# Kernel tuning notes

Hardware: AMD Instinct MI355X
Metric: run time of the kernel (lower is better)

The kernel has to match this reference:

```python
import jax, jax.numpy as jnp
import numpy as np

D_MODEL = 768
N_HEAD = 12
D_FF = 3072
EPS = 1e-5


def _layer_norm(x, w, b):
    mu = jnp.mean(x, axis=-1, keepdims=True)
    var = jnp.mean(jnp.square(x - mu), axis=-1, keepdims=True)
    return (x - mu) * jax.lax.rsqrt(var + EPS) * w + b


def setup_inputs() -> dict:
    key = jax.random.key(0)
    ks = jax.random.split(key, 8)
    B, S, D = 2, 4096, D_MODEL
    s_in = 1.0 / np.sqrt(D)
    s_ff = 1.0 / np.sqrt(D_FF)
    return {
        "src": jax.random.normal(ks[0], (B, S, D), jnp.float32),
        "w_qkv": jax.random.uniform(ks[1], (3 * D, D), jnp.float32, -s_in, s_in),
        "b_qkv": jnp.zeros((3 * D,), jnp.float32),
        "w_out": jax.random.uniform(ks[2], (D, D), jnp.float32, -s_in, s_in),
        "b_out": jnp.zeros((D,), jnp.float32),
        "w1": jax.random.uniform(ks[3], (D_FF, D), jnp.float32, -s_in, s_in),
        "b1": jnp.zeros((D_FF,), jnp.float32),
        "w2": jax.random.uniform(ks[4], (D, D_FF), jnp.float32, -s_ff, s_ff),
        "b2": jnp.zeros((D,), jnp.float32),
        "ln1_w": jnp.ones((D,), jnp.float32),
        "ln1_b": jnp.zeros((D,), jnp.float32),
        "ln2_w": jnp.ones((D,), jnp.float32),
        "ln2_b": jnp.zeros((D,), jnp.float32),
    }


def reference(src, w_qkv, b_qkv, w_out, b_out, w1, b1, w2, b2,
              ln1_w, ln1_b, ln2_w, ln2_b):
    B, S, D = src.shape
    H, dh = N_HEAD, D // N_HEAD
    # fused QKV projection: [B,S,3D]
    qkv = jnp.einsum('bsd,ed->bse', src, w_qkv) + b_qkv
    q, k, v = jnp.split(qkv, 3, axis=-1)
    q = q.reshape(B, S, H, dh)
    k = k.reshape(B, S, H, dh)
    v = v.reshape(B, S, H, dh)
    scale = 1.0 / np.sqrt(dh)
    scores = jnp.einsum('bqhd,bkhd->bhqk', q, k) * scale  # [B,H,S,S]
    attn = jax.nn.softmax(scores, axis=-1)
    ctx = jnp.einsum('bhqk,bkhd->bqhd', attn, v).reshape(B, S, D)
    attn_out = jnp.einsum('bsd,ed->bse', ctx, w_out) + b_out
    # post-norm residual (norm_first=False), dropout inactive in eval
    x = _layer_norm(src + attn_out, ln1_w, ln1_b)
    h = jax.nn.relu(jnp.einsum('bsd,fd->bsf', x, w1) + b1)
    ffn = jnp.einsum('bsf,df->bsd', h, w2) + b2
    return _layer_norm(x + ffn, ln2_w, ln2_b)
```

## Files before the change

kernel.cpp:

```cpp
#include <hip/hip_runtime.h>
#include <hip/hip_bf16.h>

typedef __hip_bfloat16 bf16;
typedef __attribute__((ext_vector_type(8))) short s16x8;
typedef __attribute__((ext_vector_type(4))) float f32x4;

#define MFMA16x16x32(A, B, C) __builtin_amdgcn_mfma_f32_16x16x32_bf16((A), (B), (C), 0, 0, 0)

__device__ __forceinline__ void async_copy16(const bf16* g, bf16* l) {
  __builtin_amdgcn_global_load_lds(
      (const __attribute__((address_space(1))) void*)g,
      (__attribute__((address_space(3))) void*)l, 16, 0, 0);
}

__device__ __forceinline__ int SW(int row, int chunk) {
  return row * 64 + (((chunk) ^ (row & 7)) << 3);
}

__global__ __launch_bounds__(256)
void cast_f2b_kernel(const float* __restrict__ in, bf16* __restrict__ out, int n) {
  const int i = (blockIdx.x * 256 + threadIdx.x) * 4;
  if (i < n) {
    const float4 f = *(const float4*)(in + i);
    out[i + 0] = (bf16)f.x; out[i + 1] = (bf16)f.y;
    out[i + 2] = (bf16)f.z; out[i + 3] = (bf16)f.w;
  }
}

template <int RELU, int VT, int ACCUM, typename OutT>
__global__ __launch_bounds__(256)
void gemm_bt_kernel(const bf16* __restrict__ A, const bf16* __restrict__ B,
                    const float* __restrict__ bias, OutT* __restrict__ C,
                    int N, int K, int ldb, bf16* __restrict__ C2) {
  __shared__ __align__(16) bf16 As[2][128 * 32];
  __shared__ __align__(16) bf16 Bs[2][128 * 32];

  const int t = threadIdx.x;
  const int lane = t & 63;
  const int wave = t >> 6;
  const int wm = (wave >> 1) << 6;
  const int wn = (wave & 1) << 6;
  const int col16 = lane & 15;
  const int quad = lane >> 4;
  const int bm = blockIdx.x;
  const int bn = blockIdx.y;

  const bf16* Ag = A + (size_t)(bm * 128 + (t >> 2)) * K + (t & 3) * 8;
  const bf16* Bg = B + (size_t)(bn * 128 + (t >> 2)) * ldb + (t & 3) * 8;

  f32x4 acc[4][4] = {};

  async_copy16(Ag, &As[0][0] + t * 8);
  async_copy16(Ag + (size_t)64 * K, &As[0][0] + 2048 + t * 8);
  async_copy16(Bg, &Bs[0][0] + t * 8);
  async_copy16(Bg + (size_t)64 * ldb, &Bs[0][0] + 2048 + t * 8);

  int n = 0;
  for (int k0 = 0; k0 < K; k0 += 32, n ^= 1) {
    __syncthreads();
    if (k0 + 32 < K) {
      const int k1 = k0 + 32;
      async_copy16(Ag + k1, &As[n ^ 1][0] + t * 8);
      async_copy16(Ag + (size_t)64 * K + k1, &As[n ^ 1][0] + 2048 + t * 8);
      async_copy16(Bg + k1, &Bs[n ^ 1][0] + t * 8);
      async_copy16(Bg + (size_t)64 * ldb + k1, &Bs[n ^ 1][0] + 2048 + t * 8);
    }
    const bf16* asn = &As[n][0];
    const bf16* bsn = &Bs[n][0];

    s16x8 af[4], bfr[4];
#pragma unroll
    for (int i = 0; i < 4; i++)
      af[i] = *(const s16x8*)(asn + (wm + i * 16 + col16) * 32 + quad * 8);
#pragma unroll
    for (int j = 0; j < 4; j++)
      bfr[j] = *(const s16x8*)(bsn + (wn + j * 16 + col16) * 32 + quad * 8);
#pragma unroll
    for (int i = 0; i < 4; i++)
#pragma unroll
      for (int j = 0; j < 4; j++)
        acc[i][j] = MFMA16x16x32(af[i], bfr[j], acc[i][j]);
  }

  const int row0 = bm * 128 + wm + quad * 4;
  const int col0 = bn * 128 + wn + col16;
#pragma unroll
  for (int j = 0; j < 4; j++) {
    const int col = col0 + j * 16;
    const float bv = ACCUM ? 0.0f : bias[col];
#pragma unroll
    for (int i = 0; i < 4; i++) {
#pragma unroll
      for (int r = 0; r < 4; r++) {
        float v = acc[i][j][r] + bv;
        if (RELU) v = fmaxf(v, 0.0f);
        const int row = row0 + i * 16 + r;
        if (VT == 1) {
          ((bf16*)C)[(size_t)((row >> 12) * 12 + (col >> 6)) * 262144 +
                     (col & 63) * 4096 + (row & 4095)] = (bf16)v;
        } else if (VT == 2) {
          if (col < 1536) {
            C[(size_t)row * N + col] = (OutT)v;
          } else {
            const int cc = col - 1536;
            C2[(size_t)((row >> 12) * 12 + (cc >> 6)) * 262144 +
               (cc & 63) * 4096 + (row & 4095)] = (bf16)v;
          }
        } else {
          const size_t idx = (size_t)row * N + col;
          if (ACCUM) v += ((const float*)C)[idx];
          C[idx] = (OutT)v;
        }
      }
    }
  }
}

__global__ __launch_bounds__(256)
void attn_kernel(const bf16* __restrict__ QK, const bf16* __restrict__ Vt,
                 bf16* __restrict__ Opart, float* __restrict__ lbuf) {
  __shared__ __align__(16) bf16 Ks[2][64 * 64];
  __shared__ __align__(16) bf16 Vs[2][64 * 64];
  __shared__ __align__(16) bf16 Ps[4][32 * 64];

  const int t = threadIdx.x, lane = t & 63, wave = t >> 6;
  const int col16 = lane & 15, quad = lane >> 4;
  const int b = blockIdx.z, h = blockIdx.y;
  const int ks = blockIdx.x >> 5;
  const int qblk = blockIdx.x & 31;
  const int qw0 = qblk * 128 + wave * 32;

  s16x8 bq[2][2];
#pragma unroll
  for (int qt = 0; qt < 2; qt++)
#pragma unroll
    for (int s = 0; s < 2; s++) {
      union { s16x8 v; bf16 hh[8]; } u;
      u.v = *(const s16x8*)(QK + (size_t)(b * 4096 + qw0 + qt * 16 + col16) * 1536 +
                            h * 64 + s * 32 + quad * 8);
#pragma unroll
      for (int e = 0; e < 8; e++) u.hh[e] = (bf16)((float)u.hh[e] * 0.18033688f);
      bq[qt][s] = u.v;
    }

  union { s16x8 v; short s_[8]; } uo1;
#pragma unroll
  for (int e = 0; e < 8; e++) uo1.s_[e] = (short)0x3F80;
  const s16x8 aones = uo1.v;

  const int srow = t >> 3;
  const int schx = (t & 7) ^ (srow & 7);
  const bf16* kgb = QK + (size_t)(b * 4096) * 1536 + 768 + h * 64;
  const bf16* vgb = Vt + (size_t)(b * 12 + h) * 262144;
  const bf16* ksrc0 = kgb + (size_t)srow * 1536 + schx * 8;
  const bf16* ksrc1 = kgb + (size_t)(32 + srow) * 1536 + schx * 8;
  const bf16* vsrc0 = vgb + (size_t)srow * 4096 + schx * 8;
  const bf16* vsrc1 = vgb + (size_t)(32 + srow) * 4096 + schx * 8;

  f32x4 o[4][2] = {};
  f32x4 lacc[2] = {};
  bf16* pw = &Ps[wave][0];

  const int kbeg = ks * 2048, kend = kbeg + 2048;

  async_copy16(ksrc0 + (size_t)kbeg * 1536, &Ks[0][0] + t * 8);
  async_copy16(ksrc1 + (size_t)kbeg * 1536, &Ks[0][0] + 2048 + t * 8);
  async_copy16(vsrc0 + kbeg, &Vs[0][0] + t * 8);
  async_copy16(vsrc1 + kbeg, &Vs[0][0] + 2048 + t * 8);

  int n = 0;
  for (int k0 = kbeg; k0 < kend; k0 += 64, n ^= 1) {
    __syncthreads();
    if (k0 + 64 < kend) {
      const int k1 = k0 + 64;
      async_copy16(ksrc0 + (size_t)k1 * 1536, &Ks[n ^ 1][0] + t * 8);
      async_copy16(ksrc1 + (size_t)k1 * 1536, &Ks[n ^ 1][0] + 2048 + t * 8);
      async_copy16(vsrc0 + k1, &Vs[n ^ 1][0] + t * 8);
      async_copy16(vsrc1 + k1, &Vs[n ^ 1][0] + 2048 + t * 8);
    }
    const bf16* ksn = &Ks[n][0];
    const bf16* vsn = &Vs[n][0];

    f32x4 st[4][2] = {};
#pragma unroll
    for (int s = 0; s < 2; s++) {
      s16x8 ak[4];
#pragma unroll
      for (int kt = 0; kt < 4; kt++)
        ak[kt] = *(const s16x8*)(ksn + SW(kt * 16 + col16, s * 4 + quad));
#pragma unroll
      for (int kt = 0; kt < 4; kt++)
#pragma unroll
        for (int qt = 0; qt < 2; qt++)
          st[kt][qt] = MFMA16x16x32(ak[kt], bq[qt][s], st[kt][qt]);
    }

#pragma unroll
    for (int qt = 0; qt < 2; qt++) {
#pragma unroll
      for (int kt = 0; kt < 4; kt++) {
        union { unsigned long long u; bf16 hh[4]; } pk;
#pragma unroll
        for (int r = 0; r < 4; r++)
          pk.hh[r] = (bf16)__builtin_amdgcn_exp2f(st[kt][qt][r]);
        *(unsigned long long*)(pw + (qt * 16 + col16) * 64 +
                               (((kt * 2 + (quad >> 1)) ^ (col16 & 7)) << 3) +
                               (quad & 1) * 4) = pk.u;
      }
    }
    asm volatile("s_waitcnt lgkmcnt(0)" ::: "memory");

#pragma unroll
    for (int s = 0; s < 2; s++) {
      s16x8 bp[2];
#pragma unroll
      for (int qt = 0; qt < 2; qt++)
        bp[qt] = *(const s16x8*)(pw + SW(qt * 16 + col16, s * 4 + quad));
#pragma unroll
      for (int qt = 0; qt < 2; qt++)
        lacc[qt] = MFMA16x16x32(aones, bp[qt], lacc[qt]);
#pragma unroll
      for (int dt = 0; dt < 4; dt++) {
        const s16x8 av = *(const s16x8*)(vsn + SW(dt * 16 + col16, s * 4 + quad));
#pragma unroll
        for (int qt = 0; qt < 2; qt++)
          o[dt][qt] = MFMA16x16x32(av, bp[qt], o[dt][qt]);
      }
    }
  }

  if (lane < 16) {
#pragma unroll
    for (int qt = 0; qt < 2; qt++)
      lbuf[(size_t)ks * 98304 + (size_t)(b * 4096 + qw0 + qt * 16 + lane) * 12 + h] =
          lacc[qt][0];
  }

#pragma unroll
  for (int qt = 0; qt < 2; qt++)
#pragma unroll
    for (int dt = 0; dt < 4; dt++)
#pragma unroll
      for (int r = 0; r < 4; r++)
        pw[(qt * 16 + col16) * 64 + (((dt * 2 + (quad >> 1)) ^ (col16 & 7)) << 3) +
           (quad & 1) * 4 + r] = (bf16)(o[dt][qt][r]);
  asm volatile("s_waitcnt lgkmcnt(0)" ::: "memory");
  const int qrow = lane >> 1, chalf = (lane & 1) * 4;
  bf16* dst = Opart + (size_t)ks * 6291456 +
              (size_t)(b * 4096 + qw0 + qrow) * 768 + h * 64 + chalf * 8;
#pragma unroll
  for (int i = 0; i < 4; i++)
    *(s16x8*)(dst + i * 8) = *(const s16x8*)(pw + SW(qrow, chalf + i));
}

__global__ __launch_bounds__(256)
void attn_combine_kernel(const bf16* __restrict__ Opart,
                         const float* __restrict__ lbuf,
                         bf16* __restrict__ ctx) {
  const int i = blockIdx.x * 256 + threadIdx.x;
  const int row = i / 96, c8 = i % 96;
  const int h = c8 >> 3;
  const float inv = 1.0f / (lbuf[(size_t)row * 12 + h] +
                            lbuf[98304 + (size_t)row * 12 + h]);
  union { s16x8 v; bf16 hh[8]; } ua, ub, uo;
  ua.v = *(const s16x8*)(Opart + (size_t)row * 768 + c8 * 8);
  ub.v = *(const s16x8*)(Opart + 6291456 + (size_t)row * 768 + c8 * 8);
#pragma unroll
  for (int j = 0; j < 8; j++)
    uo.hh[j] = (bf16)(((float)ua.hh[j] + (float)ub.hh[j]) * inv);
  *(s16x8*)(ctx + (size_t)row * 768 + c8 * 8) = uo.v;
}

__global__ __launch_bounds__(256)
void add_ln_b_kernel(const float* __restrict__ X, const float* __restrict__ Y,
                     const float* __restrict__ w, const float* __restrict__ b,
                     bf16* __restrict__ out) {
  const int row = blockIdx.x * 4 + (threadIdx.x >> 6);
  const int lane = threadIdx.x & 63;
  const float* x = X + (size_t)row * 768;
  const float* y = Y + (size_t)row * 768;
  float v[12];
  float s = 0.0f;
#pragma unroll
  for (int i = 0; i < 3; i++) {
    const int c = lane * 4 + i * 256;
    const float4 xf = *(const float4*)(x + c);
    const float4 yf = *(const float4*)(y + c);
    v[i * 4 + 0] = xf.x + yf.x; v[i * 4 + 1] = xf.y + yf.y;
    v[i * 4 + 2] = xf.z + yf.z; v[i * 4 + 3] = xf.w + yf.w;
    s += v[i * 4] + v[i * 4 + 1] + v[i * 4 + 2] + v[i * 4 + 3];
  }
#pragma unroll
  for (int off = 32; off > 0; off >>= 1) s += __shfl_xor(s, off, 64);
  const float mu = s * (1.0f / 768.0f);
  float var = 0.0f;
#pragma unroll
  for (int i = 0; i < 12; i++) { const float d = v[i] - mu; var += d * d; }
#pragma unroll
  for (int off = 32; off > 0; off >>= 1) var += __shfl_xor(var, off, 64);
  const float rs = rsqrtf(var * (1.0f / 768.0f) + 1e-5f);
#pragma unroll
  for (int i = 0; i < 12; i++) {
    const int c = lane * 4 + (i >> 2) * 256 + (i & 3);
    out[(size_t)row * 768 + c] = (bf16)((v[i] - mu) * rs * w[c] + b[c]);
  }
}

__global__ __launch_bounds__(256)
void add_ln_f_kernel(const bf16* __restrict__ X, const float* __restrict__ Y,
                     const float* __restrict__ w, const float* __restrict__ b,
                     float* __restrict__ out) {
  const int row = blockIdx.x * 4 + (threadIdx.x >> 6);
  const int lane = threadIdx.x & 63;
  const bf16* x = X + (size_t)row * 768;
  const float* y = Y + (size_t)row * 768;
  float v[12];
  float s = 0.0f;
#pragma unroll
  for (int i = 0; i < 3; i++) {
    const int c = lane * 4 + i * 256;
    const float4 yf = *(const float4*)(y + c);
    v[i * 4 + 0] = (float)x[c + 0] + yf.x; v[i * 4 + 1] = (float)x[c + 1] + yf.y;
    v[i * 4 + 2] = (float)x[c + 2] + yf.z; v[i * 4 + 3] = (float)x[c + 3] + yf.w;
    s += v[i * 4] + v[i * 4 + 1] + v[i * 4 + 2] + v[i * 4 + 3];
  }
#pragma unroll
  for (int off = 32; off > 0; off >>= 1) s += __shfl_xor(s, off, 64);
  const float mu = s * (1.0f / 768.0f);
  float var = 0.0f;
#pragma unroll
  for (int i = 0; i < 12; i++) { const float d = v[i] - mu; var += d * d; }
#pragma unroll
  for (int off = 32; off > 0; off >>= 1) var += __shfl_xor(var, off, 64);
  const float rs = rsqrtf(var * (1.0f / 768.0f) + 1e-5f);
#pragma unroll
  for (int i = 0; i < 12; i++) {
    const int c = lane * 4 + (i >> 2) * 256 + (i & 3);
    out[(size_t)row * 768 + c] = (v[i] - mu) * rs * w[c] + b[c];
  }
}

extern "C" void kernel_launch(void* const* d_in, const int* in_sizes, int n_in,
                              void* d_out, int out_size, void* d_ws, size_t ws_size,
                              hipStream_t stream) {
  (void)in_sizes; (void)n_in; (void)out_size; (void)ws_size;
  const float* src   = (const float*)d_in[0];
  const float* w_qkv = (const float*)d_in[1];
  const float* b_qkv = (const float*)d_in[2];
  const float* w_out = (const float*)d_in[3];
  const float* b_out = (const float*)d_in[4];
  const float* w1    = (const float*)d_in[5];
  const float* b1    = (const float*)d_in[6];
  const float* w2    = (const float*)d_in[7];
  const float* b2    = (const float*)d_in[8];
  const float* ln1w  = (const float*)d_in[9];
  const float* ln1b  = (const float*)d_in[10];
  const float* ln2w  = (const float*)d_in[11];
  const float* ln2b  = (const float*)d_in[12];
  float* out = (float*)d_out;

  char* ws = (char*)d_ws;
  bf16* wqkvb = (bf16*)ws;
  bf16* woutb = (bf16*)(ws + 3538944);
  bf16* w1b   = (bf16*)(ws + 4718592);
  bf16* w2b   = (bf16*)(ws + 9437184);
  bf16* srcb  = (bf16*)(ws + 14155776);
  bf16* QK    = (bf16*)(ws + 26738688);
  bf16* Vt    = (bf16*)(ws + 51904512);
  bf16* Opart = (bf16*)d_out;
  float* lbuf = (float*)ws;
  bf16* ctx   = (bf16*)(ws + 14155776);
  float* attn_out = (float*)(ws + 26738688);
  bf16* x1b   = (bf16*)(ws + 51904512);
  bf16* hbuf  = (bf16*)(ws + 14155776);
  float* ffn  = out;

  cast_f2b_kernel<<<1728, 256, 0, stream>>>(w_qkv, wqkvb, 2304 * 768);
  cast_f2b_kernel<<<576,  256, 0, stream>>>(w_out, woutb, 768 * 768);
  cast_f2b_kernel<<<2304, 256, 0, stream>>>(w1, w1b, 3072 * 768);
  cast_f2b_kernel<<<2304, 256, 0, stream>>>(w2, w2b, 768 * 3072);
  cast_f2b_kernel<<<6144, 256, 0, stream>>>(src, srcb, 8192 * 768);

  gemm_bt_kernel<0, 2, 0, bf16><<<dim3(64, 18), 256, 0, stream>>>(
      srcb, wqkvb, b_qkv, QK, 1536, 768, 768, Vt);
  attn_kernel<<<dim3(64, 12, 2), 256, 0, stream>>>(QK, Vt, Opart, lbuf);
  attn_combine_kernel<<<3072, 256, 0, stream>>>(Opart, lbuf, ctx);
  gemm_bt_kernel<0, 0, 0, float><<<dim3(64, 6), 256, 0, stream>>>(
      ctx, woutb, b_out, attn_out, 768, 768, 768, nullptr);
  add_ln_b_kernel<<<2048, 256, 0, stream>>>(src, attn_out, ln1w, ln1b, x1b);
  for (int c = 0; c < 2; c++) {
    gemm_bt_kernel<1, 0, 0, bf16><<<dim3(64, 12), 256, 0, stream>>>(
        x1b, w1b + (size_t)c * 1536 * 768, b1 + c * 1536, hbuf, 1536, 768, 768,
        nullptr);
    if (c == 0)
      gemm_bt_kernel<0, 0, 0, float><<<dim3(64, 6), 256, 0, stream>>>(
          hbuf, w2b + c * 1536, b2, ffn, 768, 1536, 3072, nullptr);
    else
      gemm_bt_kernel<0, 0, 1, float><<<dim3(64, 6), 256, 0, stream>>>(
          hbuf, w2b + c * 1536, b2, ffn, 768, 1536, 3072, nullptr);
  }
  add_ln_f_kernel<<<2048, 256, 0, stream>>>(x1b, ffn, ln2w, ln2b, out);
}
```

Before: 498.1 us.

## Enlarge attention query tile, split-K the out-projection, and merge cast launches

The attention kernel now gives each wave 64 query rows instead of 32, doubling the block's query tile to 256. Each loaded K/V tile is reused across more queries, at the cost of more registers, a larger P buffer in shared memory, and half as many blocks. The output projection is split along K into two halves written to separate buffers, which doubles its grid, and the layer-norm kernel sums both partials. The five cast kernels are fused into one launch to cut launch overhead.

```diff
diff --git a/kernel.cpp b/kernel.cpp
--- a/kernel.cpp
+++ b/kernel.cpp
@@ -18,20 +18,29 @@
 }
 
 __global__ __launch_bounds__(256)
-void cast_f2b_kernel(const float* __restrict__ in, bf16* __restrict__ out, int n) {
-  const int i = (blockIdx.x * 256 + threadIdx.x) * 4;
-  if (i < n) {
-    const float4 f = *(const float4*)(in + i);
-    out[i + 0] = (bf16)f.x; out[i + 1] = (bf16)f.y;
-    out[i + 2] = (bf16)f.z; out[i + 3] = (bf16)f.w;
-  }
+void cast_all_kernel(const float* __restrict__ s0, bf16* __restrict__ d0,
+                     const float* __restrict__ s1, bf16* __restrict__ d1,
+                     const float* __restrict__ s2, bf16* __restrict__ d2,
+                     const float* __restrict__ s3, bf16* __restrict__ d3,
+                     const float* __restrict__ s4, bf16* __restrict__ d4) {
+  int blk = blockIdx.x;
+  const float* in; bf16* out;
+  if (blk < 1728)      { in = s0; out = d0; }
+  else if (blk < 2304) { in = s1; out = d1; blk -= 1728; }
+  else if (blk < 4608) { in = s2; out = d2; blk -= 2304; }
+  else if (blk < 6912) { in = s3; out = d3; blk -= 4608; }
+  else                 { in = s4; out = d4; blk -= 6912; }
+  const int i = (blk * 256 + threadIdx.x) * 4;
+  const float4 f = *(const float4*)(in + i);
+  out[i + 0] = (bf16)f.x; out[i + 1] = (bf16)f.y;
+  out[i + 2] = (bf16)f.z; out[i + 3] = (bf16)f.w;
 }
 
 template <int RELU, int VT, int ACCUM, typename OutT>
 __global__ __launch_bounds__(256)
 void gemm_bt_kernel(const bf16* __restrict__ A, const bf16* __restrict__ B,
                     const float* __restrict__ bias, OutT* __restrict__ C,
-                    int N, int K, int ldb, bf16* __restrict__ C2) {
+                    int N, int K, int lda, int ldb, bf16* __restrict__ C2) {
   __shared__ __align__(16) bf16 As[2][128 * 32];
   __shared__ __align__(16) bf16 Bs[2][128 * 32];
 
@@ -44,14 +53,15 @@
   const int quad = lane >> 4;
   const int bm = blockIdx.x;
   const int bn = blockIdx.y;
-
-  const bf16* Ag = A + (size_t)(bm * 128 + (t >> 2)) * K + (t & 3) * 8;
-  const bf16* Bg = B + (size_t)(bn * 128 + (t >> 2)) * ldb + (t & 3) * 8;
+  const int kz = (VT == 3) ? blockIdx.z * K : 0;
+
+  const bf16* Ag = A + (size_t)(bm * 128 + (t >> 2)) * lda + (t & 3) * 8 + kz;
+  const bf16* Bg = B + (size_t)(bn * 128 + (t >> 2)) * ldb + (t & 3) * 8 + kz;
 
   f32x4 acc[4][4] = {};
 
   async_copy16(Ag, &As[0][0] + t * 8);
-  async_copy16(Ag + (size_t)64 * K, &As[0][0] + 2048 + t * 8);
+  async_copy16(Ag + (size_t)64 * lda, &As[0][0] + 2048 + t * 8);
   async_copy16(Bg, &Bs[0][0] + t * 8);
   async_copy16(Bg + (size_t)64 * ldb, &Bs[0][0] + 2048 + t * 8);
 
@@ -61,7 +71,7 @@
     if (k0 + 32 < K) {
       const int k1 = k0 + 32;
       async_copy16(Ag + k1, &As[n ^ 1][0] + t * 8);
-      async_copy16(Ag + (size_t)64 * K + k1, &As[n ^ 1][0] + 2048 + t * 8);
+      async_copy16(Ag + (size_t)64 * lda + k1, &As[n ^ 1][0] + 2048 + t * 8);
       async_copy16(Bg + k1, &Bs[n ^ 1][0] + t * 8);
       async_copy16(Bg + (size_t)64 * ldb + k1, &Bs[n ^ 1][0] + 2048 + t * 8);
     }
@@ -87,7 +97,7 @@
 #pragma unroll
   for (int j = 0; j < 4; j++) {
     const int col = col0 + j * 16;
-    const float bv = ACCUM ? 0.0f : bias[col];
+    const float bv = (ACCUM || (VT == 3 && blockIdx.z)) ? 0.0f : bias[col];
 #pragma unroll
     for (int i = 0; i < 4; i++) {
 #pragma unroll
@@ -95,10 +105,7 @@
         float v = acc[i][j][r] + bv;
         if (RELU) v = fmaxf(v, 0.0f);
         const int row = row0 + i * 16 + r;
-        if (VT == 1) {
-          ((bf16*)C)[(size_t)((row >> 12) * 12 + (col >> 6)) * 262144 +
-                     (col & 63) * 4096 + (row & 4095)] = (bf16)v;
-        } else if (VT == 2) {
+        if (VT == 2) {
           if (col < 1536) {
             C[(size_t)row * N + col] = (OutT)v;
           } else {
@@ -106,6 +113,8 @@
             C2[(size_t)((row >> 12) * 12 + (cc >> 6)) * 262144 +
                (cc & 63) * 4096 + (row & 4095)] = (bf16)v;
           }
+        } else if (VT == 3) {
+          ((float*)(blockIdx.z ? (void*)C2 : (void*)C))[(size_t)row * N + col] = v;
         } else {
           const size_t idx = (size_t)row * N + col;
           if (ACCUM) v += ((const float*)C)[idx];
@@ -116,23 +125,23 @@
   }
 }
 
-__global__ __launch_bounds__(256)
+__global__ __launch_bounds__(256, 2)
 void attn_kernel(const bf16* __restrict__ QK, const bf16* __restrict__ Vt,
                  bf16* __restrict__ Opart, float* __restrict__ lbuf) {
   __shared__ __align__(16) bf16 Ks[2][64 * 64];
   __shared__ __align__(16) bf16 Vs[2][64 * 64];
-  __shared__ __align__(16) bf16 Ps[4][32 * 64];
+  __shared__ __align__(16) bf16 Ps[4][64 * 64];
 
   const int t = threadIdx.x, lane = t & 63, wave = t >> 6;
   const int col16 = lane & 15, quad = lane >> 4;
   const int b = blockIdx.z, h = blockIdx.y;
-  const int ks = blockIdx.x >> 5;
-  const int qblk = blockIdx.x & 31;
-  const int qw0 = qblk * 128 + wave * 32;
-
-  s16x8 bq[2][2];
-#pragma unroll
-  for (int qt = 0; qt < 2; qt++)
+  const int ks = blockIdx.x >> 4;
+  const int qblk = blockIdx.x & 15;
+  const int qw0 = qblk * 256 + wave * 64;
+
+  s16x8 bq[4][2];
+#pragma unroll
+  for (int qt = 0; qt < 4; qt++)
 #pragma unroll
     for (int s = 0; s < 2; s++) {
       union { s16x8 v; bf16 hh[8]; } u;
@@ -157,8 +166,8 @@
   const bf16* vsrc0 = vgb + (size_t)srow * 4096 + schx * 8;
   const bf16* vsrc1 = vgb + (size_t)(32 + srow) * 4096 + schx * 8;
 
-  f32x4 o[4][2] = {};
-  f32x4 lacc[2] = {};
+  f32x4 o[4][4] = {};
+  f32x4 lacc[4] = {};
   bf16* pw = &Ps[wave][0];
 
   const int kbeg = ks * 2048, kend = kbeg + 2048;
@@ -181,28 +190,27 @@
     const bf16* ksn = &Ks[n][0];
     const bf16* vsn = &Vs[n][0];
 
-    f32x4 st[4][2] = {};
-#pragma unroll
-    for (int s = 0; s < 2; s++) {
-      s16x8 ak[4];
+    s16x8 ak[2][4];
+#pragma unroll
+    for (int s = 0; s < 2; s++)
 #pragma unroll
       for (int kt = 0; kt < 4; kt++)
-        ak[kt] = *(const s16x8*)(ksn + SW(kt * 16 + col16, s * 4 + quad));
-#pragma unroll
-      for (int kt = 0; kt < 4; kt++)
-#pragma unroll
-        for (int qt = 0; qt < 2; qt++)
-          st[kt][qt] = MFMA16x16x32(ak[kt], bq[qt][s], st[kt][qt]);
-    }
-
-#pragma unroll
-    for (int qt = 0; qt < 2; qt++) {
-#pragma unroll
-      for (int kt = 0; kt < 4; kt++) {
+        ak[s][kt] = *(const s16x8*)(ksn + SW(kt * 16 + col16, s * 4 + quad));
+
+#pragma unroll
+    for (int kt = 0; kt < 4; kt++) {
+      f32x4 st[4] = {};
+#pragma unroll
+      for (int s = 0; s < 2; s++)
+#pragma unroll
+        for (int qt = 0; qt < 4; qt++)
+          st[qt] = MFMA16x16x32(ak[s][kt], bq[qt][s], st[qt]);
+#pragma unroll
+      for (int qt = 0; qt < 4; qt++) {
         union { unsigned long long u; bf16 hh[4]; } pk;
 #pragma unroll
         for (int r = 0; r < 4; r++)
-          pk.hh[r] = (bf16)__builtin_amdgcn_exp2f(st[kt][qt][r]);
+          pk.hh[r] = (bf16)__builtin_amdgcn_exp2f(st[qt][r]);
         *(unsigned long long*)(pw + (qt * 16 + col16) * 64 +
                                (((kt * 2 + (quad >> 1)) ^ (col16 & 7)) << 3) +
                                (quad & 1) * 4) = pk.u;
@@ -212,18 +220,18 @@
 
 #pragma unroll
     for (int s = 0; s < 2; s++) {
-      s16x8 bp[2];
-#pragma unroll
-      for (int qt = 0; qt < 2; qt++)
+      s16x8 bp[4];
+#pragma unroll
+      for (int qt = 0; qt < 4; qt++)
         bp[qt] = *(const s16x8*)(pw + SW(qt * 16 + col16, s * 4 + quad));
 #pragma unroll
-      for (int qt = 0; qt < 2; qt++)
+      for (int qt = 0; qt < 4; qt++)
         lacc[qt] = MFMA16x16x32(aones, bp[qt], lacc[qt]);
 #pragma unroll
       for (int dt = 0; dt < 4; dt++) {
         const s16x8 av = *(const s16x8*)(vsn + SW(dt * 16 + col16, s * 4 + quad));
 #pragma unroll
-        for (int qt = 0; qt < 2; qt++)
+        for (int qt = 0; qt < 4; qt++)
           o[dt][qt] = MFMA16x16x32(av, bp[qt], o[dt][qt]);
       }
     }
@@ -231,13 +239,13 @@
 
   if (lane < 16) {
 #pragma unroll
-    for (int qt = 0; qt < 2; qt++)
+    for (int qt = 0; qt < 4; qt++)
       lbuf[(size_t)ks * 98304 + (size_t)(b * 4096 + qw0 + qt * 16 + lane) * 12 + h] =
           lacc[qt][0];
   }
 
 #pragma unroll
-  for (int qt = 0; qt < 2; qt++)
+  for (int qt = 0; qt < 4; qt++)
 #pragma unroll
     for (int dt = 0; dt < 4; dt++)
 #pragma unroll
@@ -246,11 +254,15 @@
            (quad & 1) * 4 + r] = (bf16)(o[dt][qt][r]);
   asm volatile("s_waitcnt lgkmcnt(0)" ::: "memory");
   const int qrow = lane >> 1, chalf = (lane & 1) * 4;
-  bf16* dst = Opart + (size_t)ks * 6291456 +
-              (size_t)(b * 4096 + qw0 + qrow) * 768 + h * 64 + chalf * 8;
-#pragma unroll
-  for (int i = 0; i < 4; i++)
-    *(s16x8*)(dst + i * 8) = *(const s16x8*)(pw + SW(qrow, chalf + i));
+#pragma unroll
+  for (int h2 = 0; h2 < 2; h2++) {
+    const int rl = h2 * 32 + qrow;
+    bf16* dst = Opart + (size_t)ks * 6291456 +
+                (size_t)(b * 4096 + qw0 + rl) * 768 + h * 64 + chalf * 8;
+#pragma unroll
+    for (int i = 0; i < 4; i++)
+      *(s16x8*)(dst + i * 8) = *(const s16x8*)(pw + SW(rl, chalf + i));
+  }
 }
 
 __global__ __launch_bounds__(256)
@@ -273,12 +285,14 @@
 
 __global__ __launch_bounds__(256)
 void add_ln_b_kernel(const float* __restrict__ X, const float* __restrict__ Y,
+                     const float* __restrict__ Y2,
                      const float* __restrict__ w, const float* __restrict__ b,
                      bf16* __restrict__ out) {
   const int row = blockIdx.x * 4 + (threadIdx.x >> 6);
   const int lane = threadIdx.x & 63;
   const float* x = X + (size_t)row * 768;
   const float* y = Y + (size_t)row * 768;
+  const float* y2 = Y2 + (size_t)row * 768;
   float v[12];
   float s = 0.0f;
 #pragma unroll
@@ -286,8 +300,9 @@
     const int c = lane * 4 + i * 256;
     const float4 xf = *(const float4*)(x + c);
     const float4 yf = *(const float4*)(y + c);
-    v[i * 4 + 0] = xf.x + yf.x; v[i * 4 + 1] = xf.y + yf.y;
-    v[i * 4 + 2] = xf.z + yf.z; v[i * 4 + 3] = xf.w + yf.w;
+    const float4 zf = *(const float4*)(y2 + c);
+    v[i * 4 + 0] = xf.x + yf.x + zf.x; v[i * 4 + 1] = xf.y + yf.y + zf.y;
+    v[i * 4 + 2] = xf.z + yf.z + zf.z; v[i * 4 + 3] = xf.w + yf.w + zf.w;
     s += v[i * 4] + v[i * 4 + 1] + v[i * 4 + 2] + v[i * 4 + 3];
   }
 #pragma unroll
@@ -370,34 +385,32 @@
   bf16* Opart = (bf16*)d_out;
   float* lbuf = (float*)ws;
   bf16* ctx   = (bf16*)(ws + 14155776);
-  float* attn_out = (float*)(ws + 26738688);
+  float* woP0 = (float*)(ws + 26738688);
+  float* woP1 = (float*)d_out;
   bf16* x1b   = (bf16*)(ws + 51904512);
   bf16* hbuf  = (bf16*)(ws + 14155776);
   float* ffn  = out;
 
-  cast_f2b_kernel<<<1728, 256, 0, stream>>>(w_qkv, wqkvb, 2304 * 768);
-  cast_f2b_kernel<<<576,  256, 0, stream>>>(w_out, woutb, 768 * 768);
-  cast_f2b_kernel<<<2304, 256, 0, stream>>>(w1, w1b, 3072 * 768);
-  cast_f2b_kernel<<<2304, 256, 0, stream>>>(w2, w2b, 768 * 3072);
-  cast_f2b_kernel<<<6144, 256, 0, stream>>>(src, srcb, 8192 * 768);
+  cast_all_kernel<<<13056, 256, 0, stream>>>(
+      w_qkv, wqkvb, w_out, woutb, w1, w1b, w2, w2b, src, srcb);
 
   gemm_bt_kernel<0, 2, 0, bf16><<<dim3(64, 18), 256, 0, stream>>>(
-      srcb, wqkvb, b_qkv, QK, 1536, 768, 768, Vt);
-  attn_kernel<<<dim3(64, 12, 2), 256, 0, stream>>>(QK, Vt, Opart, lbuf);
+      srcb, wqkvb, b_qkv, QK, 1536, 768, 768, 768, Vt);
+  attn_kernel<<<dim3(32, 12, 2), 256, 0, stream>>>(QK, Vt, Opart, lbuf);
   attn_combine_kernel<<<3072, 256, 0, stream>>>(Opart, lbuf, ctx);
-  gemm_bt_kernel<0, 0, 0, float><<<dim3(64, 6), 256, 0, stream>>>(
-      ctx, woutb, b_out, attn_out, 768, 768, 768, nullptr);
-  add_ln_b_kernel<<<2048, 256, 0, stream>>>(src, attn_out, ln1w, ln1b, x1b);
+  gemm_bt_kernel<0, 3, 0, float><<<dim3(64, 6, 2), 256, 0, stream>>>(
+      ctx, woutb, b_out, woP0, 768, 384, 768, 768, (bf16*)woP1);
+  add_ln_b_kernel<<<2048, 256, 0, stream>>>(src, woP0, woP1, ln1w, ln1b, x1b);
   for (int c = 0; c < 2; c++) {
     gemm_bt_kernel<1, 0, 0, bf16><<<dim3(64, 12), 256, 0, stream>>>(
         x1b, w1b + (size_t)c * 1536 * 768, b1 + c * 1536, hbuf, 1536, 768, 768,
-        nullptr);
+        768, nullptr);
     if (c == 0)
       gemm_bt_kernel<0, 0, 0, float><<<dim3(64, 6), 256, 0, stream>>>(
-          hbuf, w2b + c * 1536, b2, ffn, 768, 1536, 3072, nullptr);
+          hbuf, w2b + c * 1536, b2, ffn, 768, 1536, 1536, 3072, nullptr);
     else
       gemm_bt_kernel<0, 0, 1, float><<<dim3(64, 6), 256, 0, stream>>>(
-          hbuf, w2b + c * 1536, b2, ffn, 768, 1536, 3072, nullptr);
+          hbuf, w2b + c * 1536, b2, ffn, 768, 1536, 1536, 3072, nullptr);
   }
   add_ln_f_kernel<<<2048, 256, 0, stream>>>(x1b, ffn, ln2w, ln2b, out);
 }
```

After: 478.8 us. 1.04x faster.
